# Kernel tuning notes

Measured on AMD Instinct MI355X. Metric: run time of the kernel, lower is better.

The kernel has to match this reference:

```python
import jax, jax.numpy as jnp
import numpy as np

NUM_EMBEDDINGS = 1024
EMBEDDING_DIM = 256
COMMITMENT_COST = 0.25
DECAY = 0.99
EPSILON = 1e-5


def setup_inputs() -> dict:
    key = jax.random.key(0)
    k1, k2 = jax.random.split(key)
    B, C, D, H, W = 4, EMBEDDING_DIM, 16, 32, 32
    z = jax.random.normal(k1, (B, C, D, H, W), dtype=jnp.float32)
    bound = 1.0 / (EMBEDDING_DIM ** 0.5)  # nn.init.uniform_(-1/sqrt(d), 1/sqrt(d))
    embed = jax.random.uniform(k2, (NUM_EMBEDDINGS, EMBEDDING_DIM), dtype=jnp.float32,
                               minval=-bound, maxval=bound)
    ema_cluster_size = jnp.zeros((NUM_EMBEDDINGS,), dtype=jnp.float32)
    ema_embed_sum = embed  # buffer initialized as a clone of the embedding weight
    return {"z": z, "embed": embed,
            "ema_cluster_size": ema_cluster_size, "ema_embed_sum": ema_embed_sum}


def reference(z, embed, ema_cluster_size, ema_embed_sum):
    """Training-mode forward of VectorQuantizer (EMA codebook update included).

    Returns (z_q [B,C,D,H,W], vq_loss scalar, indices [B,D,H,W]).
    """
    K, Dm = embed.shape
    B, C, D, H, W = z.shape
    # (B,C,D,H,W) -> (B,D,H,W,C) -> (N, Dm)
    zp = jnp.transpose(z, (0, 2, 3, 4, 1))
    zf = zp.reshape(-1, Dm)

    # squared-distance via expanded cdist: |z|^2 + |e|^2 - 2 z e^T
    dist = (jnp.sum(zf * zf, axis=1, keepdims=True)
            + jnp.sum(embed * embed, axis=1)
            - 2.0 * jnp.matmul(zf, embed.T))  # (N, K)
    idx = jnp.argmin(dist, axis=1)  # (N,)

    # EMA statistics (one-hot matmuls expressed as segment sums)
    batch_cluster_size = jax.ops.segment_sum(jnp.ones_like(idx, dtype=zf.dtype), idx,
                                             num_segments=K)
    batch_embed_sum = jax.ops.segment_sum(zf, idx, num_segments=K)  # (K, Dm)
    new_ema_cs = DECAY * ema_cluster_size + (1.0 - DECAY) * batch_cluster_size
    new_ema_es = DECAY * ema_embed_sum + (1.0 - DECAY) * batch_embed_sum
    n = jnp.sum(new_ema_cs)
    cluster_size = (new_ema_cs + EPSILON) / (n + K * EPSILON) * n
    new_embed = new_ema_es / cluster_size[:, None]  # updated codebook, used for gather

    z_q = new_embed[idx].reshape(zp.shape)  # (B,D,H,W,C)
    vq_loss = COMMITMENT_COST * jnp.mean((zp - jax.lax.stop_gradient(z_q)) ** 2)
    z_q = zp + jax.lax.stop_gradient(z_q - zp)  # straight-through

    indices = idx.reshape(B, D, H, W)
    z_q = jnp.transpose(z_q, (0, 4, 1, 2, 3))  # back to (B,C,D,H,W)
    return z_q, vq_loss, indices
```

## Files before the change

### kernel.cpp

```cpp
#include <hip/hip_runtime.h>
#include <hip/hip_bf16.h>
#include <cfloat>

#define NTOT    65536
#define KCODES  1024
#define DM      256
#define SPAT    16384
#define ZQ_SIZE 16777216

#define WS_ENORM 0
#define WS_CSIZE 1024
#define WS_START 2048
#define WS_LOSSP 3104
#define WS_HIST  11296
#define WS_SORT  273440
#define WS_IDX   338976
#define WS_NEWE  404512
#define WS_BDIST 666656
#define WS_BIDX  797728

#define GLOAD_LDS16(gp, lp) __builtin_amdgcn_global_load_lds( \
    (const __attribute__((address_space(1))) unsigned int*)(gp), \
    (__attribute__((address_space(3))) unsigned int*)(lp), 16, 0, 0)

__global__ __launch_bounds__(256) void enorm_kernel(const float* __restrict__ embed,
                                                    float* __restrict__ enorm) {
    int k = blockIdx.x;
    int t = threadIdx.x;
    float v = embed[k * DM + t];
    v *= v;
    #pragma unroll
    for (int m = 32; m > 0; m >>= 1) v += __shfl_xor(v, m);
    __shared__ float sm[4];
    if ((t & 63) == 0) sm[t >> 6] = v;
    __syncthreads();
    if (t == 0) enorm[k] = sm[0] + sm[1] + sm[2] + sm[3];
}

__global__ __launch_bounds__(256, 4) void argmin_kernel(
    const float* __restrict__ z, const float* __restrict__ embed,
    const float* __restrict__ enorm, float* __restrict__ bdist,
    int* __restrict__ bidx, float* __restrict__ zt) {
    __shared__ __align__(16) float zs[2][16][64];
    __shared__ __align__(16) float es[2][128][16];

    const int tid = threadIdx.x;
    const int bx  = blockIdx.x;
    const int kh  = bx & 1;
    const int n0  = (bx >> 1) * 64;
    const int b   = n0 >> 14;
    const int s0  = n0 & 16383;
    const int ti  = tid >> 4;
    const int tj  = tid & 15;
    const int w   = tid >> 6;
    const int l   = tid & 63;

    auto stage_z = [&](int st, int buf) {
        const int c0 = (st & 15) * 16;
        int cc = c0 + w * 4 + (l >> 4);
        const float* gp = z + (size_t)(b * DM + cc) * SPAT + s0 + (l & 15) * 4;
        GLOAD_LDS16(gp, &zs[buf][w * 4][0]);
    };
    auto stage_es = [&](int st, int buf) {
        const int k0 = kh * 512 + (st >> 4) * 128;
        const int c0 = (st & 15) * 16;
        #pragma unroll
        for (int v = 0; v < 2; ++v) {
            int R = w * 32 + v * 16;
            int sg = (l & 3) ^ ((l >> 3) & 3);
            const float* gp = embed + (size_t)(k0 + R + (l >> 2)) * DM + c0 + sg * 4;
            GLOAD_LDS16(gp, &es[buf][R][0]);
        }
    };

    stage_z(0, 0);
    stage_es(0, 0);

    float best[4], acc[4][8];
    int   bestk[4];
    #pragma unroll
    for (int i = 0; i < 4; ++i) { best[i] = FLT_MAX; bestk[i] = 0; }

    #pragma unroll 1
    for (int st = 0; st < 64; ++st) {
        const int buf = st & 1;
        const int k0  = kh * 512 + (st >> 4) * 128;

        __syncthreads();

        if (st < 63) { stage_z(st + 1, buf ^ 1); stage_es(st + 1, buf ^ 1); }

        if (kh == 0 && st < 16) {
            const int c0 = st * 16;
            int r = tid >> 2, cg = tid & 3;
            float4 v4;
            v4.x = zs[buf][cg * 4 + 0][r];
            v4.y = zs[buf][cg * 4 + 1][r];
            v4.z = zs[buf][cg * 4 + 2][r];
            v4.w = zs[buf][cg * 4 + 3][r];
            *(float4*)&zt[(size_t)(n0 + r) * DM + c0 + cg * 4] = v4;
        }

        if ((st & 15) == 0) {
            #pragma unroll
            for (int i = 0; i < 4; ++i)
                #pragma unroll
                for (int j = 0; j < 8; ++j) acc[i][j] = 0.f;
        }

        #pragma unroll
        for (int cq = 0; cq < 4; ++cq) {
            float4 zq[4];
            #pragma unroll
            for (int q = 0; q < 4; ++q)
                zq[q] = *(const float4*)&zs[buf][cq * 4 + q][ti * 4];
            const int eoff = ((cq ^ ((tj >> 1) & 3)) << 2);
            #pragma unroll
            for (int j = 0; j < 8; ++j) {
                float4 eb = *(const float4*)&es[buf][tj + j * 16][eoff];
                #pragma unroll
                for (int q = 0; q < 4; ++q) {
                    float ec = (q == 0) ? eb.x : (q == 1) ? eb.y
                             : (q == 2) ? eb.z : eb.w;
                    acc[0][j] = fmaf(zq[q].x, ec, acc[0][j]);
                    acc[1][j] = fmaf(zq[q].y, ec, acc[1][j]);
                    acc[2][j] = fmaf(zq[q].z, ec, acc[2][j]);
                    acc[3][j] = fmaf(zq[q].w, ec, acc[3][j]);
                }
            }
        }

        if ((st & 15) == 15) {
            #pragma unroll
            for (int j = 0; j < 8; ++j) {
                int q = k0 + tj + j * 16;
                float en = enorm[q];
                #pragma unroll
                for (int i = 0; i < 4; ++i) {
                    float v = fmaf(-2.0f, acc[i][j], en);
                    if (v < best[i]) { best[i] = v; bestk[i] = q; }
                }
            }
        }
    }

    #pragma unroll
    for (int i = 0; i < 4; ++i) {
        float bd = best[i];
        int   bk = bestk[i];
        #pragma unroll
        for (int m = 1; m < 16; m <<= 1) {
            float od = __shfl_xor(bd, m);
            int   ok = __shfl_xor(bk, m);
            if (od < bd || (od == bd && ok < bk)) { bd = od; bk = ok; }
        }
        if (tj == 0) {
            int n = n0 + ti * 4 + i;
            bdist[kh * NTOT + n] = bd;
            bidx[kh * NTOT + n]  = bk;
        }
    }
}

__global__ __launch_bounds__(256) void merge_kernel(
    const float* __restrict__ bdist, const int* __restrict__ bidx,
    int* __restrict__ idx, float* __restrict__ dout) {
    int n = blockIdx.x * 256 + threadIdx.x;
    float d0 = bdist[n], d1 = bdist[NTOT + n];
    int k = (d1 < d0) ? bidx[NTOT + n] : bidx[n];
    idx[n] = k;
    dout[ZQ_SIZE + 1 + n] = (float)k;
}

__global__ __launch_bounds__(256) void hist_kernel(const int* __restrict__ idx,
                                                   int* __restrict__ hist) {
    __shared__ int lh[KCODES];
    int ch = blockIdx.x, t = threadIdx.x;
    #pragma unroll
    for (int u = 0; u < 4; ++u) lh[t + u * 256] = 0;
    __syncthreads();
    int k = idx[ch * 256 + t];
    atomicAdd(&lh[k], 1);
    __syncthreads();
    #pragma unroll
    for (int u = 0; u < 4; ++u)
        hist[ch * KCODES + t + u * 256] = lh[t + u * 256];
}

__global__ __launch_bounds__(1024) void scan_kernel(
    int* __restrict__ hist, const float* __restrict__ ema_cs,
    int* __restrict__ start, float* __restrict__ csize) {
    int k = threadIdx.x;
    int run = 0;
    for (int ch = 0; ch < 256; ++ch) {
        int t = hist[ch * KCODES + k];
        hist[ch * KCODES + k] = run;
        run += t;
    }
    int lane = k & 63, wv = k >> 6;
    int v = run;
    #pragma unroll
    for (int d = 1; d < 64; d <<= 1) {
        int t = __shfl_up(v, d);
        if (lane >= d) v += t;
    }
    __shared__ int wsum[16];
    if (lane == 63) wsum[wv] = v;
    __syncthreads();
    __shared__ int wpre[16];
    if (k == 0) {
        int s = 0;
        #pragma unroll
        for (int i = 0; i < 16; ++i) { wpre[i] = s; s += wsum[i]; }
    }
    __syncthreads();
    int excl = wpre[wv] + v - run;
    start[k] = excl;
    if (k == 1023) start[1024] = excl + run;
    float ncs = 0.99f * ema_cs[k] + 0.01f * (float)run;
    float r = ncs;
    #pragma unroll
    for (int m = 32; m > 0; m >>= 1) r += __shfl_xor(r, m);
    __shared__ float fs[16];
    if (lane == 0) fs[wv] = r;
    __syncthreads();
    __shared__ float nt;
    if (k == 0) {
        float s = 0.f;
        #pragma unroll
        for (int i = 0; i < 16; ++i) s += fs[i];
        nt = s;
    }
    __syncthreads();
    float n = nt;
    csize[k] = (ncs + 1e-5f) / (n + 1024.0f * 1e-5f) * n;
}

__global__ __launch_bounds__(256) void rank_scatter_kernel(
    const int* __restrict__ idx, const int* __restrict__ hist,
    const int* __restrict__ start, int* __restrict__ sorted) {
    __shared__ int lidx[256];
    int ch = blockIdx.x, t = threadIdx.x;
    int k = idx[ch * 256 + t];
    lidx[t] = k;
    __syncthreads();
    int rank = 0;
    for (int j = 0; j < 255; ++j)
        if (j < t && lidx[j] == k) ++rank;
    sorted[start[k] + hist[ch * KCODES + k] + rank] = ch * 256 + t;
}

__global__ __launch_bounds__(256) void gather_kernel(
    const float* __restrict__ zt, const int* __restrict__ sorted,
    const int* __restrict__ start, const float* __restrict__ ema_es,
    const float* __restrict__ csize, float* __restrict__ newe) {
    int k = blockIdx.x, c = threadIdx.x;
    int s0 = start[k], s1 = start[k + 1];
    float acc = 0.f;
    for (int i = s0; i < s1; ++i) {
        int n = sorted[i];
        acc += zt[(size_t)n * DM + c];
    }
    size_t o = (size_t)k * DM + c;
    newe[o] = (0.99f * ema_es[o] + 0.01f * acc) / csize[k];
}

__global__ __launch_bounds__(256) void output_kernel(
    const float* __restrict__ z, const float* __restrict__ newe,
    const int* __restrict__ idx, float* __restrict__ dout,
    float* __restrict__ lossp) {
    int gid = blockIdx.x * 256 + threadIdx.x;
    float lsum = 0.f;
    #pragma unroll
    for (int it = 0; it < 8; ++it) {
        int o = gid + it * (8192 * 256);
        int s = o & 16383, t2 = o >> 14;
        int c = t2 & 255, b = t2 >> 8;
        int n = (b << 14) + s;
        int k = idx[n];
        float v = newe[(size_t)k * DM + c];
        float zv = z[o];
        dout[o] = v;
        float d = zv - v;
        lsum = fmaf(d, d, lsum);
    }
    #pragma unroll
    for (int m = 32; m > 0; m >>= 1) lsum += __shfl_xor(lsum, m);
    __shared__ float sm[4];
    int t = threadIdx.x;
    if ((t & 63) == 0) sm[t >> 6] = lsum;
    __syncthreads();
    if (t == 0) lossp[blockIdx.x] = sm[0] + sm[1] + sm[2] + sm[3];
}

__global__ __launch_bounds__(256) void loss_final_kernel(const float* __restrict__ lossp,
                                                         float* __restrict__ dout) {
    int t = threadIdx.x;
    float v = 0.f;
    for (int i = t; i < 8192; i += 256) v += lossp[i];
    #pragma unroll
    for (int m = 32; m > 0; m >>= 1) v += __shfl_xor(v, m);
    __shared__ float sm[4];
    if ((t & 63) == 0) sm[t >> 6] = v;
    __syncthreads();
    if (t == 0) dout[ZQ_SIZE] = 0.25f * ((sm[0] + sm[1] + sm[2] + sm[3]) / 16777216.0f);
}

extern "C" void kernel_launch(void* const* d_in, const int* in_sizes, int n_in,
                              void* d_out, int out_size, void* d_ws, size_t ws_size,
                              hipStream_t stream) {
    const float* z      = (const float*)d_in[0];
    const float* embed  = (const float*)d_in[1];
    const float* ema_cs = (const float*)d_in[2];
    const float* ema_es = (const float*)d_in[3];
    float* out = (float*)d_out;
    float* ws  = (float*)d_ws;

    float* enorm = ws + WS_ENORM;
    float* csize = ws + WS_CSIZE;
    int*   start = (int*)(ws + WS_START);
    float* lossp = ws + WS_LOSSP;
    int*   hist  = (int*)(ws + WS_HIST);
    int*   sortd = (int*)(ws + WS_SORT);
    int*   idx   = (int*)(ws + WS_IDX);
    float* newe  = ws + WS_NEWE;
    float* bdist = ws + WS_BDIST;
    int*   bidx  = (int*)(ws + WS_BIDX);
    float* zt    = out;

    enorm_kernel<<<KCODES, 256, 0, stream>>>(embed, enorm);
    argmin_kernel<<<NTOT / 64 * 2, 256, 0, stream>>>(z, embed, enorm, bdist, bidx, zt);
    merge_kernel<<<NTOT / 256, 256, 0, stream>>>(bdist, bidx, idx, out);
    hist_kernel<<<256, 256, 0, stream>>>(idx, hist);
    scan_kernel<<<1, 1024, 0, stream>>>(hist, ema_cs, start, csize);
    rank_scatter_kernel<<<256, 256, 0, stream>>>(idx, hist, start, sortd);
    gather_kernel<<<KCODES, 256, 0, stream>>>(zt, sortd, start, ema_es, csize, newe);
    output_kernel<<<8192, 256, 0, stream>>>(z, newe, idx, out, lossp);
    loss_final_kernel<<<1, 256, 0, stream>>>(lossp, out);
}
```

Before: 627.0 us.

## Double the K-chunk depth per stage and remap block indices for L2 locality

Each pipeline stage of the argmin GEMM now loads 32 channels instead of 16, which halves the number of stages and their barriers. The embed tile's XOR swizzle is widened to 8 groups to match the new row width, and the stage loop is unrolled by 2. Block indices are remapped so that groups of 8 spatial tiles share the same codebook half, aiming for better cache reuse of the embed rows. The trade-off is double the LDS use per block, which may reduce how many blocks fit on each CU.

```diff
diff --git a/kernel.cpp b/kernel.cpp
--- a/kernel.cpp
+++ b/kernel.cpp
@@ -41,13 +41,13 @@
     const float* __restrict__ z, const float* __restrict__ embed,
     const float* __restrict__ enorm, float* __restrict__ bdist,
     int* __restrict__ bidx, float* __restrict__ zt) {
-    __shared__ __align__(16) float zs[2][16][64];
-    __shared__ __align__(16) float es[2][128][16];
+    __shared__ __align__(16) float zs[2][32][64];
+    __shared__ __align__(16) float es[2][128][32];
 
     const int tid = threadIdx.x;
     const int bx  = blockIdx.x;
-    const int kh  = bx & 1;
-    const int n0  = (bx >> 1) * 64;
+    const int kh  = (bx >> 3) & 1;
+    const int n0  = ((bx & 7) | ((bx >> 4) << 3)) * 64;
     const int b   = n0 >> 14;
     const int s0  = n0 & 16383;
     const int ti  = tid >> 4;
@@ -56,19 +56,23 @@
     const int l   = tid & 63;
 
     auto stage_z = [&](int st, int buf) {
-        const int c0 = (st & 15) * 16;
-        int cc = c0 + w * 4 + (l >> 4);
-        const float* gp = z + (size_t)(b * DM + cc) * SPAT + s0 + (l & 15) * 4;
-        GLOAD_LDS16(gp, &zs[buf][w * 4][0]);
+        const int c0 = (st & 7) * 32;
+        #pragma unroll
+        for (int v = 0; v < 2; ++v) {
+            int colb = w * 8 + v * 4;
+            int cc   = c0 + colb + (l >> 4);
+            const float* gp = z + (size_t)(b * DM + cc) * SPAT + s0 + (l & 15) * 4;
+            GLOAD_LDS16(gp, &zs[buf][colb][0]);
+        }
     };
     auto stage_es = [&](int st, int buf) {
-        const int k0 = kh * 512 + (st >> 4) * 128;
-        const int c0 = (st & 15) * 16;
-        #pragma unroll
-        for (int v = 0; v < 2; ++v) {
-            int R = w * 32 + v * 16;
-            int sg = (l & 3) ^ ((l >> 3) & 3);
-            const float* gp = embed + (size_t)(k0 + R + (l >> 2)) * DM + c0 + sg * 4;
+        const int k0 = kh * 512 + (st >> 3) * 128;
+        const int c0 = (st & 7) * 32;
+        #pragma unroll
+        for (int v = 0; v < 4; ++v) {
+            int R = w * 32 + v * 8;
+            int sg = (l & 7) ^ ((l >> 3) & 7);
+            const float* gp = embed + (size_t)(k0 + R + (l >> 3)) * DM + c0 + sg * 4;
             GLOAD_LDS16(gp, &es[buf][R][0]);
         }
     };
@@ -81,27 +85,32 @@
     #pragma unroll
     for (int i = 0; i < 4; ++i) { best[i] = FLT_MAX; bestk[i] = 0; }
 
-    #pragma unroll 1
-    for (int st = 0; st < 64; ++st) {
+    #pragma unroll 2
+    for (int st = 0; st < 32; ++st) {
         const int buf = st & 1;
-        const int k0  = kh * 512 + (st >> 4) * 128;
+        const int k0  = kh * 512 + (st >> 3) * 128;
 
         __syncthreads();
 
-        if (st < 63) { stage_z(st + 1, buf ^ 1); stage_es(st + 1, buf ^ 1); }
-
-        if (kh == 0 && st < 16) {
-            const int c0 = st * 16;
+        if (st < 31) { stage_z(st + 1, buf ^ 1); stage_es(st + 1, buf ^ 1); }
+
+        if (kh == 0 && st < 8) {
+            const int c0 = st * 32;
             int r = tid >> 2, cg = tid & 3;
-            float4 v4;
-            v4.x = zs[buf][cg * 4 + 0][r];
-            v4.y = zs[buf][cg * 4 + 1][r];
-            v4.z = zs[buf][cg * 4 + 2][r];
-            v4.w = zs[buf][cg * 4 + 3][r];
-            *(float4*)&zt[(size_t)(n0 + r) * DM + c0 + cg * 4] = v4;
-        }
-
-        if ((st & 15) == 0) {
+            float4 a, bv;
+            a.x  = zs[buf][cg * 8 + 0][r];
+            a.y  = zs[buf][cg * 8 + 1][r];
+            a.z  = zs[buf][cg * 8 + 2][r];
+            a.w  = zs[buf][cg * 8 + 3][r];
+            bv.x = zs[buf][cg * 8 + 4][r];
+            bv.y = zs[buf][cg * 8 + 5][r];
+            bv.z = zs[buf][cg * 8 + 6][r];
+            bv.w = zs[buf][cg * 8 + 7][r];
+            *(float4*)&zt[(size_t)(n0 + r) * DM + c0 + cg * 8] = a;
+            *(float4*)&zt[(size_t)(n0 + r) * DM + c0 + cg * 8 + 4] = bv;
+        }
+
+        if ((st & 7) == 0) {
             #pragma unroll
             for (int i = 0; i < 4; ++i)
                 #pragma unroll
@@ -109,12 +118,12 @@
         }
 
         #pragma unroll
-        for (int cq = 0; cq < 4; ++cq) {
+        for (int cq = 0; cq < 8; ++cq) {
             float4 zq[4];
             #pragma unroll
             for (int q = 0; q < 4; ++q)
                 zq[q] = *(const float4*)&zs[buf][cq * 4 + q][ti * 4];
-            const int eoff = ((cq ^ ((tj >> 1) & 3)) << 2);
+            const int eoff = ((cq ^ (tj & 7)) << 2);
             #pragma unroll
             for (int j = 0; j < 8; ++j) {
                 float4 eb = *(const float4*)&es[buf][tj + j * 16][eoff];
@@ -130,7 +139,7 @@
             }
         }
 
-        if ((st & 15) == 15) {
+        if ((st & 7) == 7) {
             #pragma unroll
             for (int j = 0; j < 8; ++j) {
                 int q = k0 + tj + j * 16;
```

Result: slower. 878.8 us (+40.2%).
